# Optimization experiments

Measured on AMD Instinct MI355X. Metric: run time of the kernel, lower is better.

## Reference

```python
import jax, jax.numpy as jnp
import numpy as np

# Dims: P patterns, L pattern length, D word dim, V vocab, H mlp hidden, C classes, N doc length
P, L, D, V, H, C, N = 256, 6, 300, 100000, 256, 5, 4096


def setup_inputs() -> dict:
    key = jax.random.key(0)
    ks = jax.random.split(key, 10)
    doc = jax.random.randint(ks[0], (N,), 0, V)
    emb = jax.random.normal(ks[1], (V, D), dtype=jnp.float32)
    diags = jax.random.normal(ks[2], (P * 2 * L, D), dtype=jnp.float32)
    diags = diags / jnp.linalg.norm(diags, axis=1, keepdims=True)  # normalize() at init
    bias = jax.random.normal(ks[3], (P * 2 * L, 1), dtype=jnp.float32)
    epsilon = jax.random.normal(ks[4], (P, L - 1), dtype=jnp.float32)
    w0 = jax.random.normal(ks[5], (H, P), dtype=jnp.float32) * 0.05
    b0 = jnp.zeros((H,), jnp.float32)
    w1 = jax.random.normal(ks[6], (H, H), dtype=jnp.float32) * 0.05
    b1 = jnp.zeros((H,), jnp.float32)
    w2 = jax.random.normal(ks[7], (C, H), dtype=jnp.float32) * 0.05
    b2 = jnp.zeros((C,), jnp.float32)
    return dict(doc=doc, emb=emb, diags=diags, bias=bias, epsilon=epsilon,
                w0=w0, b0=b0, w1=w1, b1=b1, w2=w2, b2=b2)


def reference(doc, emb, diags, bias, epsilon, w0, b0, w1, b1, w2, b2):
    # fixed scalar gates: epsilon_scale = self_loop_scale = 0.5 (non-trainable)
    sls = jax.nn.sigmoid(jnp.float32(0.5))
    eps_val = jax.nn.sigmoid(jnp.float32(0.5)) * jax.nn.sigmoid(epsilon)  # [P, L-1]

    # precompute all per-token transition matrices in one GEMM
    x = emb[doc]                                                # [N, D]
    T = jax.nn.sigmoid(x @ diags.T + bias[:, 0])                # [N, P*2*L]
    T = T.reshape(-1, P, 2, L)                                  # [N, P, 2, L]

    h0 = jnp.zeros((P, L), jnp.float32).at[:, 0].set(1.0)
    zero_pad = jnp.zeros((P, 1), jnp.float32)
    one_pad = jnp.ones((P, 1), jnp.float32)

    def step(h, Tt):  # transition_once, fused over tokens via scan
        main = jnp.concatenate([zero_pad, h[:, :-1] * Tt[:, 1, :-1]], axis=1) \
               + sls * h * Tt[:, 0, :]
        h2 = main + jnp.concatenate([one_pad, main[:, :-1] * eps_val], axis=1)
        return h2, h2[:, -1]

    _, last_states = jax.lax.scan(step, h0, T)                  # last_states: [N, P]
    scores = last_states.sum(axis=0)                            # [P]

    # MLP (num_mlp_layers=2 hidden ReLU layers, then linear to classes)
    z = scores[None, :]                                         # [1, P]
    z = jax.nn.relu(z @ w0.T + b0)
    z = jax.nn.relu(z @ w1.T + b1)
    return z @ w2.T + b2                                        # [1, C]
```

## Files before the change

kernel.cpp:

```cpp
#include <hip/hip_runtime.h>
#include <hip/hip_bf16.h>
#include <cstdint>
#include <cstddef>

#define P_ 256
#define L_ 6
#define D_ 300
#define J_ 3072
#define N_ 4096
#define H_ 256
#define C_ 5
#define KP 320
#define KSTEPS 10

#define SLS 0.62245933120185459f

typedef __attribute__((ext_vector_type(8))) short short8v;
typedef __attribute__((ext_vector_type(4))) short short4v;
typedef __attribute__((ext_vector_type(4))) float f32x4;

__device__ __forceinline__ float sigmoidf_(float x) { return 1.0f / (1.0f + __expf(-x)); }
__device__ __forceinline__ float bf2f(short s) { return __uint_as_float(((unsigned)(unsigned short)s) << 16); }
__device__ __forceinline__ short f2bf(float f) {
    __hip_bfloat16 h = __float2bfloat16(f);
    return *reinterpret_cast<const short*>(&h);
}

__global__ __launch_bounds__(256) void prep_XB(
    const int* __restrict__ doc, const float* __restrict__ emb,
    const float* __restrict__ diags,
    __hip_bfloat16* __restrict__ X, __hip_bfloat16* __restrict__ Bb)
{
    const int i = blockIdx.x * 256 + threadIdx.x;
    const int NX4 = N_ * (KP / 4);
    float4 v = {0.f, 0.f, 0.f, 0.f};
    if (i < NX4) {
        const int n = i / (KP / 4), k4 = i - n * (KP / 4);
        if (k4 < D_ / 4)
            v = ((const float4*)(emb + (size_t)doc[n] * D_))[k4];
        short4v pk = { f2bf(v.x), f2bf(v.y), f2bf(v.z), f2bf(v.w) };
        *(short4v*)(X + (size_t)i * 4) = pk;
    } else {
        const int ii = i - NX4;
        const int j = ii / (KP / 4), k4 = ii - j * (KP / 4);
        if (k4 < D_ / 4)
            v = ((const float4*)(diags + (size_t)j * D_))[k4];
        short4v pk = { f2bf(v.x), f2bf(v.y), f2bf(v.z), f2bf(v.w) };
        *(short4v*)(Bb + (size_t)ii * 4) = pk;
    }
}

__global__ __launch_bounds__(256) void gemm_mfma(
    const __hip_bfloat16* __restrict__ X, const __hip_bfloat16* __restrict__ Bb,
    const float* __restrict__ bias, __hip_bfloat16* __restrict__ Tt)
{
    __shared__ __hip_bfloat16 As[2][128 * 32];
    __shared__ __hip_bfloat16 Bs[2][128 * 32];

    const int tid  = threadIdx.x;
    const int lane = tid & 63;
    const int w    = tid >> 6;
    const int wr   = w >> 1, wc = w & 1;

    const int bid = blockIdx.x;
    const int swz = (bid & 7) * 96 + (bid >> 3);
    const int bx  = swz % 24, by = swz / 24;
    const int m0  = by * 128;
    const int j0  = bx * 128;

    const int srow = w * 32 + (lane >> 2);
    const int scol = (lane & 3) * 8;

    f32x4 acc[4][4];
    #pragma unroll
    for (int m = 0; m < 4; ++m)
        #pragma unroll
        for (int n = 0; n < 4; ++n)
            acc[m][n] = (f32x4){0.f, 0.f, 0.f, 0.f};

    const int fr = lane & 15;
    const int kg = (lane >> 4) * 8;

    auto stage = [&](int kt, int b) {
        const int k0 = kt * 32;
        #pragma unroll
        for (int q = 0; q < 2; ++q) {
            const __hip_bfloat16* ga = X + (size_t)(m0 + srow + q * 16) * KP + k0 + scol;
            __builtin_amdgcn_global_load_lds(
                (const __attribute__((address_space(1))) unsigned*)ga,
                (__attribute__((address_space(3))) unsigned*)(&As[b][(w * 2 + q) * 512]),
                16, 0, 0);
            const __hip_bfloat16* gb = Bb + (size_t)(j0 + srow + q * 16) * KP + k0 + scol;
            __builtin_amdgcn_global_load_lds(
                (const __attribute__((address_space(1))) unsigned*)gb,
                (__attribute__((address_space(3))) unsigned*)(&Bs[b][(w * 2 + q) * 512]),
                16, 0, 0);
        }
    };

    stage(0, 0);
    __syncthreads();

    int buf = 0;
    for (int kt = 0; kt < KSTEPS; ++kt) {
        if (kt + 1 < KSTEPS) stage(kt + 1, buf ^ 1);

        short8v a[4], b[4];
        #pragma unroll
        for (int m = 0; m < 4; ++m)
            a[m] = *(const short8v*)(&As[buf][(wr * 64 + m * 16 + fr) * 32 + kg]);
        #pragma unroll
        for (int n = 0; n < 4; ++n)
            b[n] = *(const short8v*)(&Bs[buf][(wc * 64 + n * 16 + fr) * 32 + kg]);
        #pragma unroll
        for (int m = 0; m < 4; ++m)
            #pragma unroll
            for (int n = 0; n < 4; ++n)
                acc[m][n] = __builtin_amdgcn_mfma_f32_16x16x32_bf16(a[m], b[n], acc[m][n], 0, 0, 0);

        __syncthreads();
        buf ^= 1;
    }

    #pragma unroll
    for (int n = 0; n < 4; ++n) {
        const int j = j0 + wc * 64 + n * 16 + fr;
        const float bj = bias[j];
        #pragma unroll
        for (int m = 0; m < 4; ++m) {
            const int rbase = m0 + wr * 64 + m * 16 + (lane >> 4) * 4;
            short4v pk;
            #pragma unroll
            for (int r = 0; r < 4; ++r)
                pk[r] = f2bf(sigmoidf_(acc[m][n][r] + bj));
            *(short4v*)(Tt + (size_t)j * N_ + rbase) = pk;
        }
    }
}

__device__ __forceinline__ void compose_maps(const float* C, const float* R, float* N)
{
    #pragma unroll
    for (int j = 0; j < 7; ++j) {
        #pragma unroll
        for (int i = 0; i < 6; ++i) {
            float a = (j == 6) ? C[42 + i] : 0.0f;
            #pragma unroll
            for (int u = 0; u < 6; ++u) a = fmaf(C[u * 7 + i], R[j * 7 + u], a);
            N[j * 7 + i] = a;
        }
        float sa = R[j * 7 + 6] + ((j == 6) ? C[48] : 0.0f);
        #pragma unroll
        for (int u = 0; u < 6; ++u) sa = fmaf(C[u * 7 + 6], R[j * 7 + u], sa);
        N[j * 7 + 6] = sa;
    }
}

__global__ __launch_bounds__(256) void scan_tree(
    const __hip_bfloat16* __restrict__ Tt, const float* __restrict__ epsilon,
    float* __restrict__ scores)
{
    __shared__ float lds[256 * 49];
    const int tid = threadIdx.x;
    const int p   = blockIdx.x;

    {
        const int c = tid;
        float ep[5];
        #pragma unroll
        for (int l = 0; l < 5; ++l)
            ep[l] = SLS * (1.0f / (1.0f + __expf(-epsilon[p * 5 + l])));

        float hc[7][6], sc[7];
        #pragma unroll
        for (int j = 0; j < 7; ++j) {
            sc[j] = 0.0f;
            #pragma unroll
            for (int i = 0; i < 6; ++i) hc[j][i] = (i == j) ? 1.0f : 0.0f;
        }

        #pragma unroll
        for (int h = 0; h < 2; ++h) {
            short8v v[12];
            #pragma unroll
            for (int l = 0; l < 12; ++l)
                v[l] = *(const short8v*)(Tt + (size_t)(p * 12 + l) * N_ + c * 16 + h * 8);

            #pragma unroll
            for (int tt = 0; tt < 8; ++tt) {
                float sT0[6], T1v[6];
                #pragma unroll
                for (int l = 0; l < 6; ++l) {
                    sT0[l] = SLS * bf2f(v[l][tt]);
                    T1v[l] = bf2f(v[6 + l][tt]);
                }
                #pragma unroll
                for (int j = 0; j < 7; ++j) {
                    float m[6];
                    m[0] = hc[j][0] * sT0[0];
                    #pragma unroll
                    for (int i = 1; i < 6; ++i)
                        m[i] = fmaf(hc[j][i - 1], T1v[i - 1], hc[j][i] * sT0[i]);
                    hc[j][0] = m[0] + ((j == 6) ? 1.0f : 0.0f);
                    #pragma unroll
                    for (int i = 1; i < 6; ++i)
                        hc[j][i] = fmaf(m[i - 1], ep[i - 1], m[i]);
                    sc[j] += hc[j][5];
                }
            }
        }

        #pragma unroll
        for (int j = 0; j < 7; ++j) {
            #pragma unroll
            for (int i = 0; i < 6; ++i) lds[c * 49 + j * 7 + i] = hc[j][i];
            lds[c * 49 + j * 7 + 6] = sc[j];
        }
    }

    for (int act = 128; act >= 1; act >>= 1) {
        __syncthreads();
        float Nn[49];
        const bool on = (tid < act);
        if (on) compose_maps(&lds[(2 * tid + 1) * 49], &lds[(2 * tid) * 49], Nn);
        __syncthreads();
        if (on) {
            #pragma unroll
            for (int q = 0; q < 49; ++q) lds[tid * 49 + q] = Nn[q];
        }
    }

    if (tid == 0) scores[p] = lds[6] + lds[48];
}

__global__ __launch_bounds__(1024) void mlp_head(
    const float* __restrict__ scores,
    const float* __restrict__ w0, const float* __restrict__ b0,
    const float* __restrict__ w1, const float* __restrict__ b1,
    const float* __restrict__ w2, const float* __restrict__ b2,
    float* __restrict__ out)
{
    __shared__ float s0[H_], z0[H_], z1[H_];
    __shared__ float part[1024];
    const int tid = threadIdx.x;
    const int r = tid >> 2;
    const int q = tid & 3;

    if (tid < P_) s0[tid] = scores[tid];
    __syncthreads();

    {
        const float4* wr = (const float4*)(w0 + (size_t)r * P_ + q * 64);
        float sum = 0.f;
        #pragma unroll
        for (int k = 0; k < 16; ++k) {
            float4 wv = wr[k];
            const float* sv = &s0[q * 64 + k * 4];
            sum = fmaf(wv.x, sv[0], sum);
            sum = fmaf(wv.y, sv[1], sum);
            sum = fmaf(wv.z, sv[2], sum);
            sum = fmaf(wv.w, sv[3], sum);
        }
        part[tid] = sum;
    }
    __syncthreads();
    if (tid < H_) {
        float s = part[4 * tid] + part[4 * tid + 1] + part[4 * tid + 2] + part[4 * tid + 3];
        z0[tid] = fmaxf(s + b0[tid], 0.f);
    }
    __syncthreads();

    {
        const float4* wr = (const float4*)(w1 + (size_t)r * H_ + q * 64);
        float sum = 0.f;
        #pragma unroll
        for (int k = 0; k < 16; ++k) {
            float4 wv = wr[k];
            const float* sv = &z0[q * 64 + k * 4];
            sum = fmaf(wv.x, sv[0], sum);
            sum = fmaf(wv.y, sv[1], sum);
            sum = fmaf(wv.z, sv[2], sum);
            sum = fmaf(wv.w, sv[3], sum);
        }
        part[tid] = sum;
    }
    __syncthreads();
    if (tid < H_) {
        float s = part[4 * tid] + part[4 * tid + 1] + part[4 * tid + 2] + part[4 * tid + 3];
        z1[tid] = fmaxf(s + b1[tid], 0.f);
    }
    __syncthreads();

    if (tid < C_ * 64) {
        const int rr = tid >> 6, u = tid & 63;
        float4 wv = ((const float4*)(w2 + (size_t)rr * H_))[u];
        const float* sv = &z1[u * 4];
        float sum = wv.x * sv[0] + wv.y * sv[1] + wv.z * sv[2] + wv.w * sv[3];
        #pragma unroll
        for (int msk = 32; msk >= 1; msk >>= 1) sum += __shfl_xor(sum, msk, 64);
        if (u == 0) out[rr] = sum + b2[rr];
    }
}

extern "C" void kernel_launch(void* const* d_in, const int* in_sizes, int n_in,
                              void* d_out, int out_size, void* d_ws, size_t ws_size,
                              hipStream_t stream)
{
    const int*   doc     = (const int*)d_in[0];
    const float* emb     = (const float*)d_in[1];
    const float* diags   = (const float*)d_in[2];
    const float* bias    = (const float*)d_in[3];
    const float* epsilon = (const float*)d_in[4];
    const float* w0      = (const float*)d_in[5];
    const float* b0      = (const float*)d_in[6];
    const float* w1      = (const float*)d_in[7];
    const float* b1      = (const float*)d_in[8];
    const float* w2      = (const float*)d_in[9];
    const float* b2      = (const float*)d_in[10];
    float* out = (float*)d_out;

    float* scores = (float*)d_ws;
    __hip_bfloat16* Tt = (__hip_bfloat16*)((float*)d_ws + 512);
    __hip_bfloat16* X  = Tt + (size_t)J_ * N_;
    __hip_bfloat16* Bb = X  + (size_t)N_ * KP;

    prep_XB<<<(N_ * KP + J_ * KP) / 1024, 256, 0, stream>>>(doc, emb, diags, X, Bb);
    gemm_mfma<<<(J_ / 128) * (N_ / 128), 256, 0, stream>>>(X, Bb, bias, Tt);
    scan_tree<<<P_, 256, 0, stream>>>(Tt, epsilon, scores);
    mlp_head<<<1, 1024, 0, stream>>>(scores, w0, b0, w1, b1, w2, b2, out);
}
```

Baseline: 64.01 us.

## Fuse embedding gather and bf16 conversion into the MFMA GEMM loader

Removes the separate prep kernel that gathered embedding rows and converted emb/diags to padded bf16 buffers. The GEMM now loads fp32 rows directly from emb (indexed through doc) and diags into LDS with async global-to-LDS loads and an XOR-swizzled layout, zero-fills the K tail past 300, and converts to bf16 in registers before the MFMA. This drops one launch and a write-then-read round trip through global memory. In exchange LDS traffic and footprint double, each k-step does extra conversion ALU work, and the fp32 rows (stride 300) may not give aligned 16-byte loads as cleanly.

```diff
diff --git a/kernel.cpp b/kernel.cpp
--- a/kernel.cpp
+++ b/kernel.cpp
@@ -10,7 +10,6 @@
 #define N_ 4096
 #define H_ 256
 #define C_ 5
-#define KP 320
 #define KSTEPS 10
 
 #define SLS 0.62245933120185459f
@@ -26,36 +25,13 @@
     return *reinterpret_cast<const short*>(&h);
 }
 
-__global__ __launch_bounds__(256) void prep_XB(
+__global__ __launch_bounds__(256) void gemm_fp32d(
     const int* __restrict__ doc, const float* __restrict__ emb,
-    const float* __restrict__ diags,
-    __hip_bfloat16* __restrict__ X, __hip_bfloat16* __restrict__ Bb)
-{
-    const int i = blockIdx.x * 256 + threadIdx.x;
-    const int NX4 = N_ * (KP / 4);
-    float4 v = {0.f, 0.f, 0.f, 0.f};
-    if (i < NX4) {
-        const int n = i / (KP / 4), k4 = i - n * (KP / 4);
-        if (k4 < D_ / 4)
-            v = ((const float4*)(emb + (size_t)doc[n] * D_))[k4];
-        short4v pk = { f2bf(v.x), f2bf(v.y), f2bf(v.z), f2bf(v.w) };
-        *(short4v*)(X + (size_t)i * 4) = pk;
-    } else {
-        const int ii = i - NX4;
-        const int j = ii / (KP / 4), k4 = ii - j * (KP / 4);
-        if (k4 < D_ / 4)
-            v = ((const float4*)(diags + (size_t)j * D_))[k4];
-        short4v pk = { f2bf(v.x), f2bf(v.y), f2bf(v.z), f2bf(v.w) };
-        *(short4v*)(Bb + (size_t)ii * 4) = pk;
-    }
-}
-
-__global__ __launch_bounds__(256) void gemm_mfma(
-    const __hip_bfloat16* __restrict__ X, const __hip_bfloat16* __restrict__ Bb,
-    const float* __restrict__ bias, __hip_bfloat16* __restrict__ Tt)
-{
-    __shared__ __hip_bfloat16 As[2][128 * 32];
-    __shared__ __hip_bfloat16 Bs[2][128 * 32];
+    const float* __restrict__ diags, const float* __restrict__ bias,
+    __hip_bfloat16* __restrict__ Tt)
+{
+    __shared__ float As[2][4096];
+    __shared__ float Bs[2][4096];
 
     const int tid  = threadIdx.x;
     const int lane = tid & 63;
@@ -68,8 +44,37 @@
     const int m0  = by * 128;
     const int j0  = bx * 128;
 
-    const int srow = w * 32 + (lane >> 2);
-    const int scol = (lane & 3) * 8;
+    const int hrow = lane >> 3;
+    const int sblk = (lane & 7) ^ hrow;
+    int rloc[4], drow[4];
+    #pragma unroll
+    for (int q = 0; q < 4; ++q) {
+        rloc[q] = w * 32 + q * 8 + hrow;
+        drow[q] = doc[m0 + rloc[q]];
+    }
+
+    auto stage = [&](int kt, int b) {
+        const int k0 = kt * 32;
+        const bool tail = (kt == KSTEPS - 1);
+        #pragma unroll
+        for (int q = 0; q < 4; ++q) {
+            float* dstA = &As[b][w * 1024 + q * 256 + lane * 4];
+            float* dstB = &Bs[b][w * 1024 + q * 256 + lane * 4];
+            if (!tail || sblk < 3) {
+                const float* ga = emb + (size_t)drow[q] * D_ + k0 + sblk * 4;
+                __builtin_amdgcn_global_load_lds(
+                    (const __attribute__((address_space(1))) unsigned*)ga,
+                    (__attribute__((address_space(3))) unsigned*)dstA, 16, 0, 0);
+                const float* gb = diags + (size_t)(j0 + rloc[q]) * D_ + k0 + sblk * 4;
+                __builtin_amdgcn_global_load_lds(
+                    (const __attribute__((address_space(1))) unsigned*)gb,
+                    (__attribute__((address_space(3))) unsigned*)dstB, 16, 0, 0);
+            } else {
+                *(f32x4*)dstA = (f32x4){0.f, 0.f, 0.f, 0.f};
+                *(f32x4*)dstB = (f32x4){0.f, 0.f, 0.f, 0.f};
+            }
+        }
+    };
 
     f32x4 acc[4][4];
     #pragma unroll
@@ -79,24 +84,10 @@
             acc[m][n] = (f32x4){0.f, 0.f, 0.f, 0.f};
 
     const int fr = lane & 15;
-    const int kg = (lane >> 4) * 8;
-
-    auto stage = [&](int kt, int b) {
-        const int k0 = kt * 32;
-        #pragma unroll
-        for (int q = 0; q < 2; ++q) {
-            const __hip_bfloat16* ga = X + (size_t)(m0 + srow + q * 16) * KP + k0 + scol;
-            __builtin_amdgcn_global_load_lds(
-                (const __attribute__((address_space(1))) unsigned*)ga,
-                (__attribute__((address_space(3))) unsigned*)(&As[b][(w * 2 + q) * 512]),
-                16, 0, 0);
-            const __hip_bfloat16* gb = Bb + (size_t)(j0 + srow + q * 16) * KP + k0 + scol;
-            __builtin_amdgcn_global_load_lds(
-                (const __attribute__((address_space(1))) unsigned*)gb,
-                (__attribute__((address_space(3))) unsigned*)(&Bs[b][(w * 2 + q) * 512]),
-                16, 0, 0);
-        }
-    };
+    const int kq = lane >> 4;
+    const int f7 = fr & 7;
+    const int s0 = ((2 * kq)     ^ f7) * 4;
+    const int s1 = ((2 * kq + 1) ^ f7) * 4;
 
     stage(0, 0);
     __syncthreads();
@@ -107,11 +98,25 @@
 
         short8v a[4], b[4];
         #pragma unroll
-        for (int m = 0; m < 4; ++m)
-            a[m] = *(const short8v*)(&As[buf][(wr * 64 + m * 16 + fr) * 32 + kg]);
-        #pragma unroll
-        for (int n = 0; n < 4; ++n)
-            b[n] = *(const short8v*)(&Bs[buf][(wc * 64 + n * 16 + fr) * 32 + kg]);
+        for (int m = 0; m < 4; ++m) {
+            const int ra = (wr * 64 + m * 16 + fr) * 32;
+            f32x4 lo = *(const f32x4*)(&As[buf][ra + s0]);
+            f32x4 hi = *(const f32x4*)(&As[buf][ra + s1]);
+            short8v v;
+            #pragma unroll
+            for (int e = 0; e < 4; ++e) { v[e] = f2bf(lo[e]); v[4 + e] = f2bf(hi[e]); }
+            a[m] = v;
+        }
+        #pragma unroll
+        for (int n = 0; n < 4; ++n) {
+            const int rb = (wc * 64 + n * 16 + fr) * 32;
+            f32x4 lo = *(const f32x4*)(&Bs[buf][rb + s0]);
+            f32x4 hi = *(const f32x4*)(&Bs[buf][rb + s1]);
+            short8v v;
+            #pragma unroll
+            for (int e = 0; e < 4; ++e) { v[e] = f2bf(lo[e]); v[4 + e] = f2bf(hi[e]); }
+            b[n] = v;
+        }
         #pragma unroll
         for (int m = 0; m < 4; ++m)
             #pragma unroll
@@ -321,11 +326,8 @@
 
     float* scores = (float*)d_ws;
     __hip_bfloat16* Tt = (__hip_bfloat16*)((float*)d_ws + 512);
-    __hip_bfloat16* X  = Tt + (size_t)J_ * N_;
-    __hip_bfloat16* Bb = X  + (size_t)N_ * KP;
-
-    prep_XB<<<(N_ * KP + J_ * KP) / 1024, 256, 0, stream>>>(doc, emb, diags, X, Bb);
-    gemm_mfma<<<(J_ / 128) * (N_ / 128), 256, 0, stream>>>(X, Bb, bias, Tt);
+
+    gemm_fp32d<<<(J_ / 128) * (N_ / 128), 256, 0, stream>>>(doc, emb, diags, bias, Tt);
     scan_tree<<<P_, 256, 0, stream>>>(Tt, epsilon, scores);
     mlp_head<<<1, 1024, 0, stream>>>(scores, w0, b0, w1, b1, w2, b2, out);
 }
```

Result: slower. 73.31 us (+14.5%).
